# Performance work log

Measured on AMD Instinct MI355X. Metric: run time of the kernel, lower is better.

Reference implementation:

```python
import jax, jax.numpy as jnp
import numpy as np

N = 100000
NCLASS = 64
E = 1600000
NHID = 256
TOPK = 16
DEGREE = 9


def setup_inputs() -> dict:
    key = jax.random.key(0)
    ks = jax.random.split(key, 10)
    return {
        "f_prediction": jax.random.normal(ks[0], (N, NCLASS), dtype=jnp.float32),
        "g0_prediction": jax.random.normal(ks[1], (N, NCLASS), dtype=jnp.float32),
        "adj_rows": jax.random.randint(ks[2], (E,), 0, N, dtype=jnp.int32),
        "adj_cols": jax.random.randint(ks[3], (E,), 0, N, dtype=jnp.int32),
        "adj_vals": jax.random.uniform(ks[4], (E,), dtype=jnp.float32) / 16.0,
        "W1": jax.random.normal(ks[5], (TOPK, 2 * NHID), dtype=jnp.float32) * 0.1,
        "b1": jnp.zeros((2 * NHID,), dtype=jnp.float32),
        "W2": jax.random.normal(ks[6], (2 * NHID, NHID), dtype=jnp.float32) * 0.1,
        "b2": jnp.zeros((NHID,), dtype=jnp.float32),
        "W3": jax.random.normal(ks[7], (NHID, DEGREE), dtype=jnp.float32) * 0.1,
        "b3": jnp.zeros((DEGREE,), dtype=jnp.float32),
    }


def spmm(rows, cols, vals, x):
    # out[i] = sum_{e: rows[e]==i} vals[e] * x[cols[e]]
    msgs = vals[:, None] * x[cols]  # [E, F]
    return jax.ops.segment_sum(msgs, rows, num_segments=N)


def reference(f_prediction, g0_prediction, adj_rows, adj_cols, adj_vals,
              W1, b1, W2, b2, W3, b3):
    g0 = jax.nn.softmax(g0_prediction, axis=1)
    ranked, _ = jax.lax.top_k(g0, TOPK)  # [N, TOPK], sorted descending
    h = jnp.tanh(ranked @ W1 + b1)
    h = jnp.tanh(h @ W2 + b2)
    weight = h @ W3 + b3  # [N, DEGREE]

    f = f_prediction
    final = weight[:, 0:1] * f
    for i in range(DEGREE - 1):
        f = spmm(adj_rows, adj_cols, adj_vals, f)
        final = final + weight[:, i + 1:i + 2] * f
    return jax.nn.log_softmax(final, axis=1), weight
```

## Files before the change

### kernel.cpp

```cpp
#include <hip/hip_runtime.h>
#include <hip/hip_bf16.h>

#define N_NODES 100000
#define NCLASS  64
#define NEDGE   1600000
#define NHID    256
#define TOPK    16
#define DEGREE  9

#define TM 32
#define H2PAD (NHID + 4)

typedef __attribute__((ext_vector_type(8))) short bf16x8;
typedef __attribute__((ext_vector_type(4))) float f32x4;

__device__ __forceinline__ float fast_tanh(float x) {
    float e = __expf(2.0f * x);
    return 1.0f - 2.0f / (e + 1.0f);
}

__device__ __forceinline__ ushort bf16_hi(float x) {
    uint u = __float_as_uint(x);
    uint r = (u + 0x7FFFu + ((u >> 16) & 1u)) >> 16;
    return (ushort)r;
}
__device__ __forceinline__ float bf16_tof(ushort h) {
    return __uint_as_float(((uint)h) << 16);
}


__global__ void hist_kernel(const int* __restrict__ rows, int* __restrict__ counts, int e) {
    for (int i = blockIdx.x * blockDim.x + threadIdx.x; i < e; i += gridDim.x * blockDim.x)
        atomicAdd(&counts[rows[i]], 1);
}

__global__ __launch_bounds__(1024) void scan_blocks(const int* __restrict__ counts,
                                                    int* __restrict__ partial,
                                                    int* __restrict__ blocksums, int n) {
    __shared__ int s[1024];
    int tid = threadIdx.x;
    int gid = blockIdx.x * 1024 + tid;
    int v = (gid < n) ? counts[gid] : 0;
    s[tid] = v;
    __syncthreads();
    for (int off = 1; off < 1024; off <<= 1) {
        int t = (tid >= off) ? s[tid - off] : 0;
        __syncthreads();
        s[tid] += t;
        __syncthreads();
    }
    if (gid < n) partial[gid] = s[tid] - v;
    if (tid == 1023) blocksums[blockIdx.x] = s[1023];
}

__global__ void scan_sums(int* __restrict__ blocksums, int nb) {
    if (blockIdx.x == 0 && threadIdx.x == 0) {
        int run = 0;
        for (int i = 0; i < nb; ++i) { int v = blocksums[i]; blocksums[i] = run; run += v; }
    }
}

__global__ void finalize_rows(const int* __restrict__ partial, const int* __restrict__ blocksums,
                              int* __restrict__ row_start, int* __restrict__ cursor, int n, int e) {
    int i = blockIdx.x * blockDim.x + threadIdx.x;
    if (i < n) {
        int v = partial[i] + blocksums[i >> 10];
        row_start[i] = v;
        cursor[i] = v;
    }
    if (i == 0) row_start[n] = e;
}

__global__ void scatter_edges(const int* __restrict__ rows, const int* __restrict__ cols,
                              const float* __restrict__ vals, int* __restrict__ cursor,
                              int2* __restrict__ sedge, int e) {
    for (int i = blockIdx.x * blockDim.x + threadIdx.x; i < e; i += gridDim.x * blockDim.x) {
        int r = rows[i];
        int pos = atomicAdd(&cursor[r], 1);
        sedge[pos] = make_int2(cols[i], __float_as_int(vals[i]));
    }
}


__global__ __launch_bounds__(256) void softmax_topk(const float* __restrict__ g0,
                                                    float* __restrict__ ranked, int n) {
    int wave = (blockIdx.x * 256 + threadIdx.x) >> 6;
    int lane = threadIdx.x & 63;
    if (wave >= n) return;
    float x = g0[(size_t)wave * NCLASS + lane];
    float m = x;
    #pragma unroll
    for (int o = 1; o < 64; o <<= 1) m = fmaxf(m, __shfl_xor(m, o));
    float p = expf(x - m);
    float s = p;
    #pragma unroll
    for (int o = 1; o < 64; o <<= 1) s += __shfl_xor(s, o);
    p /= s;
    float v = p;
    #pragma unroll
    for (int k = 2; k <= 64; k <<= 1) {
        #pragma unroll
        for (int j = k >> 1; j > 0; j >>= 1) {
            float o = __shfl_xor(v, j);
            bool up = (lane & k) != 0;
            bool takeMax = (((lane & j) == 0) != up);
            v = takeMax ? fmaxf(v, o) : fminf(v, o);
        }
    }
    if (lane < TOPK) ranked[wave * TOPK + lane] = v;
}


__global__ __launch_bounds__(256) void w2frag_build(const float* __restrict__ W2,
                                                    ushort* __restrict__ fhi,
                                                    ushort* __restrict__ flo) {
    int idx = blockIdx.x * 256 + threadIdx.x;
    if (idx >= 16 * 16 * 64) return;
    int l = idx & 63;
    int tile = idx >> 6;
    int nt = tile & 15, ks = tile >> 4;
    int col = nt * 16 + (l & 15);
    int krow = ks * 32 + (l >> 4) * 8;
    #pragma unroll
    for (int j = 0; j < 8; ++j) {
        float wv = W2[(size_t)(krow + j) * NHID + col];
        ushort h = bf16_hi(wv);
        float res = wv - bf16_tof(h);
        fhi[(size_t)idx * 8 + j] = h;
        flo[(size_t)idx * 8 + j] = bf16_hi(res);
    }
}


__global__ __launch_bounds__(256) void mlp_kernel(const float* __restrict__ ranked,
                                                  const float* __restrict__ W1, const float* __restrict__ b1,
                                                  const ushort* __restrict__ w2fh,
                                                  const ushort* __restrict__ w2fl,
                                                  const float* __restrict__ b2,
                                                  const float* __restrict__ W3, const float* __restrict__ b3,
                                                  float* __restrict__ weight_out, int n) {
    __shared__ float s_rank[TM][TOPK];
    __shared__ ushort s_h1[2][TM][2 * NHID];
    float (*s_h2)[H2PAD] = reinterpret_cast<float (*)[H2PAD]>(&s_h1[0][0][0]);

    const int t = threadIdx.x;
    const int row0 = blockIdx.x * TM;
    char* h1base = reinterpret_cast<char*>(&s_h1[0][0][0]);
    const uint LOBYTES = TM * 2 * NHID * 2;

    for (int idx = t; idx < TM * TOPK; idx += 256) {
        int r = idx >> 4, k = idx & 15;
        int gr = row0 + r;
        s_rank[r][k] = (gr < n) ? ranked[gr * TOPK + k] : 0.0f;
    }
    __syncthreads();

    {
        float w1a[TOPK], w1b[TOPK];
        #pragma unroll
        for (int k = 0; k < TOPK; ++k) {
            w1a[k] = W1[k * (2 * NHID) + t];
            w1b[k] = W1[k * (2 * NHID) + t + NHID];
        }
        float ba = b1[t], bb = b1[t + NHID];
        for (int r = 0; r < TM; ++r) {
            float4 q0 = *reinterpret_cast<const float4*>(&s_rank[r][0]);
            float4 q1 = *reinterpret_cast<const float4*>(&s_rank[r][4]);
            float4 q2 = *reinterpret_cast<const float4*>(&s_rank[r][8]);
            float4 q3 = *reinterpret_cast<const float4*>(&s_rank[r][12]);
            float rk[TOPK] = {q0.x, q0.y, q0.z, q0.w, q1.x, q1.y, q1.z, q1.w,
                              q2.x, q2.y, q2.z, q2.w, q3.x, q3.y, q3.z, q3.w};
            float a = ba, b = bb;
            #pragma unroll
            for (int k = 0; k < TOPK; ++k) {
                a = fmaf(rk[k], w1a[k], a);
                b = fmaf(rk[k], w1b[k], b);
            }
            float ha = fast_tanh(a), hb = fast_tanh(b);
            ushort hah = bf16_hi(ha);
            ushort hal = bf16_hi(ha - bf16_tof(hah));
            ushort hbh = bf16_hi(hb);
            ushort hbl = bf16_hi(hb - bf16_tof(hbh));
            uint swz = (uint)(r & 7) << 4;
            uint offa = ((uint)(r * 1024 + t * 2)) ^ swz;
            uint offb = ((uint)(r * 1024 + (t + NHID) * 2)) ^ swz;
            *reinterpret_cast<ushort*>(h1base + offa) = hah;
            *reinterpret_cast<ushort*>(h1base + LOBYTES + offa) = hal;
            *reinterpret_cast<ushort*>(h1base + offb) = hbh;
            *reinterpret_cast<ushort*>(h1base + LOBYTES + offb) = hbl;
        }
    }
    __syncthreads();

    const int w = t >> 6, l = t & 63;
    const int mt = w & 1;
    const int nt0 = (w >> 1) * 8;
    f32x4 acc[8];
    #pragma unroll
    for (int nn = 0; nn < 8; ++nn) {
        float bv = b2[(nt0 + nn) * 16 + (l & 15)];
        acc[nn] = (f32x4){bv, bv, bv, bv};
    }
    const int arow = mt * 16 + (l & 15);
    const uint aswz = (uint)(arow & 7) << 4;
    for (int ks = 0; ks < 16; ++ks) {
        uint aoff = ((uint)(arow * 1024 + ks * 64 + (l >> 4) * 16)) ^ aswz;
        bf16x8 ah = *reinterpret_cast<const bf16x8*>(h1base + aoff);
        bf16x8 al = *reinterpret_cast<const bf16x8*>(h1base + LOBYTES + aoff);
        #pragma unroll
        for (int nn = 0; nn < 8; ++nn) {
            size_t boff = (size_t)(((ks * 16 + nt0 + nn) * 64 + l)) * 8;
            bf16x8 bh = *reinterpret_cast<const bf16x8*>(w2fh + boff);
            bf16x8 bl = *reinterpret_cast<const bf16x8*>(w2fl + boff);
            acc[nn] = __builtin_amdgcn_mfma_f32_16x16x32_bf16(ah, bh, acc[nn], 0, 0, 0);
            acc[nn] = __builtin_amdgcn_mfma_f32_16x16x32_bf16(ah, bl, acc[nn], 0, 0, 0);
            acc[nn] = __builtin_amdgcn_mfma_f32_16x16x32_bf16(al, bh, acc[nn], 0, 0, 0);
        }
    }
    __syncthreads();

    #pragma unroll
    for (int nn = 0; nn < 8; ++nn) {
        #pragma unroll
        for (int i = 0; i < 4; ++i) {
            int rr = mt * 16 + (l >> 4) * 4 + i;
            int cc = (nt0 + nn) * 16 + (l & 15);
            s_h2[rr][cc] = fast_tanh(acc[nn][i]);
        }
    }
    __syncthreads();

    for (int idx = t; idx < TM * DEGREE; idx += 256) {
        int r = idx / DEGREE, d = idx % DEGREE;
        float a3 = b3[d];
        for (int k = 0; k < NHID; k += 4) {
            float4 h = *reinterpret_cast<const float4*>(&s_h2[r][k]);
            a3 = fmaf(h.x, W3[(k + 0) * DEGREE + d], a3);
            a3 = fmaf(h.y, W3[(k + 1) * DEGREE + d], a3);
            a3 = fmaf(h.z, W3[(k + 2) * DEGREE + d], a3);
            a3 = fmaf(h.w, W3[(k + 3) * DEGREE + d], a3);
        }
        int gr = row0 + r;
        if (gr < n) weight_out[gr * DEGREE + d] = a3;
    }
}


__global__ void init_final(const float* __restrict__ fpred, const float* __restrict__ weight,
                           float* __restrict__ finalbuf, int n) {
    int i = blockIdx.x * blockDim.x + threadIdx.x;
    if (i < n * NCLASS) {
        int row = i >> 6;
        finalbuf[i] = weight[row * DEGREE] * fpred[i];
    }
}

__global__ __launch_bounds__(256) void spmm_fused(const int* __restrict__ row_start,
                                                  const int2* __restrict__ sedge,
                                                  const float* __restrict__ x,
                                                  float* __restrict__ y,
                                                  const float* __restrict__ weight,
                                                  float* __restrict__ finalbuf,
                                                  int wcol, int n) {
    int wave = (blockIdx.x * 256 + threadIdx.x) >> 6;
    int lane = threadIdx.x & 63;
    if (wave >= n) return;
    int e0 = row_start[wave], e1 = row_start[wave + 1];
    float a[8] = {0.0f, 0.0f, 0.0f, 0.0f, 0.0f, 0.0f, 0.0f, 0.0f};
    for (int e = e0; e < e1; e += 8) {
        int2 dd[8];
        #pragma unroll
        for (int i = 0; i < 8; ++i) {
            int ei = (e + i < e1) ? (e + i) : (e1 - 1);
            dd[i] = sedge[ei];
        }
        float xv[8];
        #pragma unroll
        for (int i = 0; i < 8; ++i)
            xv[i] = x[(size_t)dd[i].x * NCLASS + lane];
        #pragma unroll
        for (int i = 0; i < 8; ++i) {
            float v = (e + i < e1) ? __int_as_float(dd[i].y) : 0.0f;
            a[i] = fmaf(v, xv[i], a[i]);
        }
    }
    float acc = ((a[0] + a[1]) + (a[2] + a[3])) + ((a[4] + a[5]) + (a[6] + a[7]));
    int o = wave * NCLASS + lane;
    y[o] = acc;
    finalbuf[o] += weight[wave * DEGREE + wcol] * acc;
}

__global__ __launch_bounds__(256) void logsoftmax_inplace(float* __restrict__ out, int n) {
    int wave = (blockIdx.x * 256 + threadIdx.x) >> 6;
    int lane = threadIdx.x & 63;
    if (wave >= n) return;
    int o = wave * NCLASS + lane;
    float x = out[o];
    float m = x;
    #pragma unroll
    for (int off = 1; off < 64; off <<= 1) m = fmaxf(m, __shfl_xor(m, off));
    float p = expf(x - m);
    float s = p;
    #pragma unroll
    for (int off = 1; off < 64; off <<= 1) s += __shfl_xor(s, off);
    out[o] = x - m - logf(s);
}


extern "C" void kernel_launch(void* const* d_in, const int* in_sizes, int n_in,
                              void* d_out, int out_size, void* d_ws, size_t ws_size,
                              hipStream_t stream) {
    const float* f_pred = (const float*)d_in[0];
    const float* g0     = (const float*)d_in[1];
    const int*   arows  = (const int*)d_in[2];
    const int*   acols  = (const int*)d_in[3];
    const float* avals  = (const float*)d_in[4];
    const float* W1     = (const float*)d_in[5];
    const float* b1     = (const float*)d_in[6];
    const float* W2     = (const float*)d_in[7];
    const float* b2     = (const float*)d_in[8];
    const float* W3     = (const float*)d_in[9];
    const float* b3     = (const float*)d_in[10];

    float* out_ls = (float*)d_out;
    float* weight = (float*)d_out + (size_t)N_NODES * NCLASS;

    char* ws = (char*)d_ws;
    size_t off = 0;
    auto alloc = [&](size_t bytes) {
        void* p = ws + off;
        off += (bytes + 255) & ~(size_t)255;
        return p;
    };
    float*  ranked    = (float*)alloc((size_t)N_NODES * TOPK * 4);
    float*  fA        = (float*)alloc((size_t)N_NODES * NCLASS * 4);
    float*  fB        = (float*)alloc((size_t)N_NODES * NCLASS * 4);
    int*    counts    = (int*)alloc((size_t)N_NODES * 4);
    int*    partial   = (int*)alloc((size_t)N_NODES * 4);
    int*    row_start = (int*)alloc((size_t)(N_NODES + 1) * 4);
    int*    cursor    = (int*)alloc((size_t)N_NODES * 4);
    int*    blocksums = (int*)alloc(128 * 4);
    ushort* w2fh      = (ushort*)alloc((size_t)16 * 16 * 64 * 8 * 2);
    ushort* w2fl      = (ushort*)alloc((size_t)16 * 16 * 64 * 8 * 2);
    int2*   sedge     = (int2*)alloc((size_t)NEDGE * 8);

    const int SCAN_BLOCKS = (N_NODES + 1023) / 1024;

    hipMemsetAsync(counts, 0, (size_t)N_NODES * 4, stream);
    hist_kernel<<<2048, 256, 0, stream>>>(arows, counts, NEDGE);
    scan_blocks<<<SCAN_BLOCKS, 1024, 0, stream>>>(counts, partial, blocksums, N_NODES);
    scan_sums<<<1, 64, 0, stream>>>(blocksums, SCAN_BLOCKS);
    finalize_rows<<<(N_NODES + 255) / 256, 256, 0, stream>>>(partial, blocksums, row_start, cursor,
                                                             N_NODES, NEDGE);
    scatter_edges<<<2048, 256, 0, stream>>>(arows, acols, avals, cursor, sedge, NEDGE);

    w2frag_build<<<64, 256, 0, stream>>>(W2, w2fh, w2fl);
    softmax_topk<<<(N_NODES + 3) / 4, 256, 0, stream>>>(g0, ranked, N_NODES);
    mlp_kernel<<<(N_NODES + TM - 1) / TM, 256, 0, stream>>>(ranked, W1, b1, w2fh, w2fl, b2,
                                                            W3, b3, weight, N_NODES);

    init_final<<<(N_NODES * NCLASS + 255) / 256, 256, 0, stream>>>(f_pred, weight, out_ls, N_NODES);

    const float* xin = f_pred;
    float* bufs[2] = {fA, fB};
    for (int it = 0; it < DEGREE - 1; ++it) {
        float* y = bufs[it & 1];
        spmm_fused<<<(N_NODES + 3) / 4, 256, 0, stream>>>(row_start, sedge, xin, y, weight, out_ls,
                                                          it + 1, N_NODES);
        xin = y;
    }

    logsoftmax_inplace<<<(N_NODES + 3) / 4, 256, 0, stream>>>(out_ls, N_NODES);
}
```

Baseline: 1.291 ms.

## Fuse init and log-softmax into SpMM passes, prescale columns, pipeline MLP loads

The separate init_final and logsoftmax kernels are folded into the first and last SpMM launches via a templated mode, so the final buffer takes fewer full passes and the last SpMM skips writing y. Edge column indices are pre-multiplied by NCLASS at scatter time. The SpMM gather now uses an unpredicated 16-wide batch with 8-wide and scalar tails instead of clamped 8-wide batches. The MLP kernel gets vectorized W1/b1 loads with packed LDS stores, double-buffered register prefetch of W2 fragments across k-steps, and a transposed W3 for float4 loads. These add register pressure in the MLP and SpMM kernels.

```diff
diff --git a/kernel.cpp b/kernel.cpp
--- a/kernel.cpp
+++ b/kernel.cpp
@@ -77,7 +77,7 @@
     for (int i = blockIdx.x * blockDim.x + threadIdx.x; i < e; i += gridDim.x * blockDim.x) {
         int r = rows[i];
         int pos = atomicAdd(&cursor[r], 1);
-        sedge[pos] = make_int2(cols[i], __float_as_int(vals[i]));
+        sedge[pos] = make_int2(cols[i] * NCLASS, __float_as_int(vals[i]));
     }
 }
 
@@ -131,13 +131,21 @@
     }
 }
 
+__global__ void w3t_build(const float* __restrict__ W3, float* __restrict__ W3t) {
+    int i = blockIdx.x * 256 + threadIdx.x;
+    if (i < NHID * DEGREE) {
+        int d = i / NHID, k = i % NHID;
+        W3t[d * NHID + k] = W3[k * DEGREE + d];
+    }
+}
+
 
 __global__ __launch_bounds__(256) void mlp_kernel(const float* __restrict__ ranked,
                                                   const float* __restrict__ W1, const float* __restrict__ b1,
                                                   const ushort* __restrict__ w2fh,
                                                   const ushort* __restrict__ w2fl,
                                                   const float* __restrict__ b2,
-                                                  const float* __restrict__ W3, const float* __restrict__ b3,
+                                                  const float* __restrict__ W3t, const float* __restrict__ b3,
                                                   float* __restrict__ weight_out, int n) {
     __shared__ float s_rank[TM][TOPK];
     __shared__ ushort s_h1[2][TM][2 * NHID];
@@ -159,10 +167,10 @@
         float w1a[TOPK], w1b[TOPK];
         #pragma unroll
         for (int k = 0; k < TOPK; ++k) {
-            w1a[k] = W1[k * (2 * NHID) + t];
-            w1b[k] = W1[k * (2 * NHID) + t + NHID];
+            float2 wv = *reinterpret_cast<const float2*>(&W1[k * (2 * NHID) + 2 * t]);
+            w1a[k] = wv.x; w1b[k] = wv.y;
         }
-        float ba = b1[t], bb = b1[t + NHID];
+        float2 b12 = *reinterpret_cast<const float2*>(&b1[2 * t]);
         for (int r = 0; r < TM; ++r) {
             float4 q0 = *reinterpret_cast<const float4*>(&s_rank[r][0]);
             float4 q1 = *reinterpret_cast<const float4*>(&s_rank[r][4]);
@@ -170,7 +178,7 @@
             float4 q3 = *reinterpret_cast<const float4*>(&s_rank[r][12]);
             float rk[TOPK] = {q0.x, q0.y, q0.z, q0.w, q1.x, q1.y, q1.z, q1.w,
                               q2.x, q2.y, q2.z, q2.w, q3.x, q3.y, q3.z, q3.w};
-            float a = ba, b = bb;
+            float a = b12.x, b = b12.y;
             #pragma unroll
             for (int k = 0; k < TOPK; ++k) {
                 a = fmaf(rk[k], w1a[k], a);
@@ -181,13 +189,9 @@
             ushort hal = bf16_hi(ha - bf16_tof(hah));
             ushort hbh = bf16_hi(hb);
             ushort hbl = bf16_hi(hb - bf16_tof(hbh));
-            uint swz = (uint)(r & 7) << 4;
-            uint offa = ((uint)(r * 1024 + t * 2)) ^ swz;
-            uint offb = ((uint)(r * 1024 + (t + NHID) * 2)) ^ swz;
-            *reinterpret_cast<ushort*>(h1base + offa) = hah;
-            *reinterpret_cast<ushort*>(h1base + LOBYTES + offa) = hal;
-            *reinterpret_cast<ushort*>(h1base + offb) = hbh;
-            *reinterpret_cast<ushort*>(h1base + LOBYTES + offb) = hbl;
+            uint offa = ((uint)(r * 1024 + t * 4)) ^ ((uint)(r & 7) << 4);
+            *reinterpret_cast<uint*>(h1base + offa) = (uint)hah | ((uint)hbh << 16);
+            *reinterpret_cast<uint*>(h1base + LOBYTES + offa) = (uint)hal | ((uint)hbl << 16);
         }
     }
     __syncthreads();
@@ -203,20 +207,44 @@
     }
     const int arow = mt * 16 + (l & 15);
     const uint aswz = (uint)(arow & 7) << 4;
-    for (int ks = 0; ks < 16; ++ks) {
-        uint aoff = ((uint)(arow * 1024 + ks * 64 + (l >> 4) * 16)) ^ aswz;
-        bf16x8 ah = *reinterpret_cast<const bf16x8*>(h1base + aoff);
-        bf16x8 al = *reinterpret_cast<const bf16x8*>(h1base + LOBYTES + aoff);
-        #pragma unroll
-        for (int nn = 0; nn < 8; ++nn) {
-            size_t boff = (size_t)(((ks * 16 + nt0 + nn) * 64 + l)) * 8;
-            bf16x8 bh = *reinterpret_cast<const bf16x8*>(w2fh + boff);
-            bf16x8 bl = *reinterpret_cast<const bf16x8*>(w2fl + boff);
-            acc[nn] = __builtin_amdgcn_mfma_f32_16x16x32_bf16(ah, bh, acc[nn], 0, 0, 0);
-            acc[nn] = __builtin_amdgcn_mfma_f32_16x16x32_bf16(ah, bl, acc[nn], 0, 0, 0);
-            acc[nn] = __builtin_amdgcn_mfma_f32_16x16x32_bf16(al, bh, acc[nn], 0, 0, 0);
-        }
-    }
+    const uint abase = (uint)(arow * 1024 + (l >> 4) * 16);
+    const ushort* bhp = w2fh + (size_t)nt0 * 512 + (size_t)l * 8;
+    const ushort* blp = w2fl + (size_t)nt0 * 512 + (size_t)l * 8;
+
+    bf16x8 bAh[8], bAl[8], bBh[8], bBl[8];
+    #pragma unroll
+    for (int nn = 0; nn < 8; ++nn) {
+        bAh[nn] = *reinterpret_cast<const bf16x8*>(bhp + nn * 512);
+        bAl[nn] = *reinterpret_cast<const bf16x8*>(blp + nn * 512);
+    }
+
+#define L2STEP(CURH, CURL, NXTH, NXTL, KS)                                             \
+    {                                                                                  \
+        uint aoff = (abase + (uint)(KS) * 64) ^ aswz;                                  \
+        bf16x8 ah = *reinterpret_cast<const bf16x8*>(h1base + aoff);                   \
+        bf16x8 al = *reinterpret_cast<const bf16x8*>(h1base + LOBYTES + aoff);         \
+        if ((KS) < 15) {                                                               \
+            const ushort* ph = bhp + (size_t)((KS) + 1) * 8192;                        \
+            const ushort* pl = blp + (size_t)((KS) + 1) * 8192;                        \
+            _Pragma("unroll")                                                          \
+            for (int nn = 0; nn < 8; ++nn) {                                           \
+                NXTH[nn] = *reinterpret_cast<const bf16x8*>(ph + nn * 512);            \
+                NXTL[nn] = *reinterpret_cast<const bf16x8*>(pl + nn * 512);            \
+            }                                                                          \
+        }                                                                              \
+        _Pragma("unroll")                                                              \
+        for (int nn = 0; nn < 8; ++nn) {                                               \
+            acc[nn] = __builtin_amdgcn_mfma_f32_16x16x32_bf16(ah, CURH[nn], acc[nn], 0, 0, 0); \
+            acc[nn] = __builtin_amdgcn_mfma_f32_16x16x32_bf16(ah, CURL[nn], acc[nn], 0, 0, 0); \
+            acc[nn] = __builtin_amdgcn_mfma_f32_16x16x32_bf16(al, CURH[nn], acc[nn], 0, 0, 0); \
+        }                                                                              \
+    }
+
+    for (int ks = 0; ks < 16; ks += 2) {
+        L2STEP(bAh, bAl, bBh, bBl, ks)
+        L2STEP(bBh, bBl, bAh, bAl, ks + 1)
+    }
+#undef L2STEP
     __syncthreads();
 
     #pragma unroll
@@ -232,13 +260,15 @@
 
     for (int idx = t; idx < TM * DEGREE; idx += 256) {
         int r = idx / DEGREE, d = idx % DEGREE;
+        const float* wt = W3t + d * NHID;
         float a3 = b3[d];
         for (int k = 0; k < NHID; k += 4) {
             float4 h = *reinterpret_cast<const float4*>(&s_h2[r][k]);
-            a3 = fmaf(h.x, W3[(k + 0) * DEGREE + d], a3);
-            a3 = fmaf(h.y, W3[(k + 1) * DEGREE + d], a3);
-            a3 = fmaf(h.z, W3[(k + 2) * DEGREE + d], a3);
-            a3 = fmaf(h.w, W3[(k + 3) * DEGREE + d], a3);
+            float4 wv = *reinterpret_cast<const float4*>(&wt[k]);
+            a3 = fmaf(h.x, wv.x, a3);
+            a3 = fmaf(h.y, wv.y, a3);
+            a3 = fmaf(h.z, wv.z, a3);
+            a3 = fmaf(h.w, wv.w, a3);
         }
         int gr = row0 + r;
         if (gr < n) weight_out[gr * DEGREE + d] = a3;
@@ -246,64 +276,67 @@
 }
 
 
-__global__ void init_final(const float* __restrict__ fpred, const float* __restrict__ weight,
-                           float* __restrict__ finalbuf, int n) {
-    int i = blockIdx.x * blockDim.x + threadIdx.x;
-    if (i < n * NCLASS) {
-        int row = i >> 6;
-        finalbuf[i] = weight[row * DEGREE] * fpred[i];
-    }
-}
-
+template<int MODE>
 __global__ __launch_bounds__(256) void spmm_fused(const int* __restrict__ row_start,
                                                   const int2* __restrict__ sedge,
                                                   const float* __restrict__ x,
                                                   float* __restrict__ y,
                                                   const float* __restrict__ weight,
                                                   float* __restrict__ finalbuf,
+                                                  const float* __restrict__ fpred,
                                                   int wcol, int n) {
-    int wave = (blockIdx.x * 256 + threadIdx.x) >> 6;
+    int row = (blockIdx.x * 256 + threadIdx.x) >> 6;
     int lane = threadIdx.x & 63;
-    if (wave >= n) return;
-    int e0 = row_start[wave], e1 = row_start[wave + 1];
-    float a[8] = {0.0f, 0.0f, 0.0f, 0.0f, 0.0f, 0.0f, 0.0f, 0.0f};
-    for (int e = e0; e < e1; e += 8) {
-        int2 dd[8];
-        #pragma unroll
-        for (int i = 0; i < 8; ++i) {
-            int ei = (e + i < e1) ? (e + i) : (e1 - 1);
-            dd[i] = sedge[ei];
-        }
+    if (row >= n) return;
+    int e0 = row_start[row], e1 = row_start[row + 1];
+    float a[16];
+    #pragma unroll
+    for (int i = 0; i < 16; ++i) a[i] = 0.0f;
+    int e = e0;
+    for (; e + 15 < e1; e += 16) {
+        int2 d[16];
+        #pragma unroll
+        for (int i = 0; i < 16; ++i) d[i] = sedge[e + i];
+        float xv[16];
+        #pragma unroll
+        for (int i = 0; i < 16; ++i) xv[i] = x[(uint)d[i].x + lane];
+        #pragma unroll
+        for (int i = 0; i < 16; ++i) a[i] = fmaf(__int_as_float(d[i].y), xv[i], a[i]);
+    }
+    for (; e + 7 < e1; e += 8) {
+        int2 d[8];
+        #pragma unroll
+        for (int i = 0; i < 8; ++i) d[i] = sedge[e + i];
         float xv[8];
         #pragma unroll
-        for (int i = 0; i < 8; ++i)
-            xv[i] = x[(size_t)dd[i].x * NCLASS + lane];
-        #pragma unroll
-        for (int i = 0; i < 8; ++i) {
-            float v = (e + i < e1) ? __int_as_float(dd[i].y) : 0.0f;
-            a[i] = fmaf(v, xv[i], a[i]);
-        }
-    }
-    float acc = ((a[0] + a[1]) + (a[2] + a[3])) + ((a[4] + a[5]) + (a[6] + a[7]));
-    int o = wave * NCLASS + lane;
-    y[o] = acc;
-    finalbuf[o] += weight[wave * DEGREE + wcol] * acc;
-}
-
-__global__ __launch_bounds__(256) void logsoftmax_inplace(float* __restrict__ out, int n) {
-    int wave = (blockIdx.x * 256 + threadIdx.x) >> 6;
-    int lane = threadIdx.x & 63;
-    if (wave >= n) return;
-    int o = wave * NCLASS + lane;
-    float x = out[o];
-    float m = x;
-    #pragma unroll
-    for (int off = 1; off < 64; off <<= 1) m = fmaxf(m, __shfl_xor(m, off));
-    float p = expf(x - m);
-    float s = p;
-    #pragma unroll
-    for (int off = 1; off < 64; off <<= 1) s += __shfl_xor(s, off);
-    out[o] = x - m - logf(s);
+        for (int i = 0; i < 8; ++i) xv[i] = x[(uint)d[i].x + lane];
+        #pragma unroll
+        for (int i = 0; i < 8; ++i) a[i] = fmaf(__int_as_float(d[i].y), xv[i], a[i]);
+    }
+    for (; e < e1; ++e) {
+        int2 d = sedge[e];
+        a[0] = fmaf(__int_as_float(d.y), x[(uint)d.x + lane], a[0]);
+    }
+    float acc = (((a[0] + a[1]) + (a[2] + a[3])) + ((a[4] + a[5]) + (a[6] + a[7])))
+              + (((a[8] + a[9]) + (a[10] + a[11])) + ((a[12] + a[13]) + (a[14] + a[15])));
+    int o = row * NCLASS + lane;
+    if (MODE == 0) {
+        y[o] = acc;
+        finalbuf[o] = weight[row * DEGREE] * fpred[o] + weight[row * DEGREE + 1] * acc;
+    } else if (MODE == 1) {
+        y[o] = acc;
+        finalbuf[o] += weight[row * DEGREE + wcol] * acc;
+    } else {
+        float v = finalbuf[o] + weight[row * DEGREE + (DEGREE - 1)] * acc;
+        float m = v;
+        #pragma unroll
+        for (int off = 1; off < 64; off <<= 1) m = fmaxf(m, __shfl_xor(m, off));
+        float p = expf(v - m);
+        float s = p;
+        #pragma unroll
+        for (int off = 1; off < 64; off <<= 1) s += __shfl_xor(s, off);
+        finalbuf[o] = v - m - logf(s);
+    }
 }
 
 
@@ -342,6 +375,7 @@
     int*    blocksums = (int*)alloc(128 * 4);
     ushort* w2fh      = (ushort*)alloc((size_t)16 * 16 * 64 * 8 * 2);
     ushort* w2fl      = (ushort*)alloc((size_t)16 * 16 * 64 * 8 * 2);
+    float*  W3t       = (float*)alloc((size_t)DEGREE * NHID * 4);
     int2*   sedge     = (int2*)alloc((size_t)NEDGE * 8);
 
     const int SCAN_BLOCKS = (N_NODES + 1023) / 1024;
@@ -355,20 +389,25 @@
     scatter_edges<<<2048, 256, 0, stream>>>(arows, acols, avals, cursor, sedge, NEDGE);
 
     w2frag_build<<<64, 256, 0, stream>>>(W2, w2fh, w2fl);
+    w3t_build<<<(NHID * DEGREE + 255) / 256, 256, 0, stream>>>(W3, W3t);
     softmax_topk<<<(N_NODES + 3) / 4, 256, 0, stream>>>(g0, ranked, N_NODES);
     mlp_kernel<<<(N_NODES + TM - 1) / TM, 256, 0, stream>>>(ranked, W1, b1, w2fh, w2fl, b2,
-                                                            W3, b3, weight, N_NODES);
-
-    init_final<<<(N_NODES * NCLASS + 255) / 256, 256, 0, stream>>>(f_pred, weight, out_ls, N_NODES);
-
+                                                            W3t, b3, weight, N_NODES);
+
+    const int SPMM_BLOCKS = (N_NODES + 3) / 4;
     const float* xin = f_pred;
     float* bufs[2] = {fA, fB};
     for (int it = 0; it < DEGREE - 1; ++it) {
         float* y = bufs[it & 1];
-        spmm_fused<<<(N_NODES + 3) / 4, 256, 0, stream>>>(row_start, sedge, xin, y, weight, out_ls,
-                                                          it + 1, N_NODES);
+        if (it == 0)
+            spmm_fused<0><<<SPMM_BLOCKS, 256, 0, stream>>>(row_start, sedge, xin, y, weight,
+                                                           out_ls, f_pred, 1, N_NODES);
+        else if (it < DEGREE - 2)
+            spmm_fused<1><<<SPMM_BLOCKS, 256, 0, stream>>>(row_start, sedge, xin, y, weight,
+                                                           out_ls, nullptr, it + 1, N_NODES);
+        else
+            spmm_fused<2><<<SPMM_BLOCKS, 256, 0, stream>>>(row_start, sedge, xin, y, weight,
+                                                           out_ls, nullptr, it + 1, N_NODES);
         xin = y;
     }
-
-    logsoftmax_inplace<<<(N_NODES + 3) / 4, 256, 0, stream>>>(out_ls, N_NODES);
-}
+}
```

Result: faster. 1.216 ms (-5.8%).
